# Optimization experiments

Measured on AMD Instinct MI355X. Metric: run time of the kernel, lower is better.

Reference implementation:

```python
import jax, jax.numpy as jnp
import numpy as np


def setup_inputs() -> dict:
    key = jax.random.key(0)
    k1, k2, k3 = jax.random.split(key, 3)
    batch, h, num_logical, n_pairs = 2048, 128, 64, 512
    # P: (batch, h, h) soft assignment (approximately doubly stochastic via row softmax)
    P = jax.nn.softmax(jax.random.uniform(k1, (batch, h, h), dtype=jnp.float32) * 4.0, axis=-1)
    # d_error: (h, h) precomputed nonnegative error-distance matrix, symmetric w/ zero diag
    d = jax.random.uniform(k2, (h, h), dtype=jnp.float32)
    d_error = (d + d.T) * (1.0 - jnp.eye(h, dtype=jnp.float32))
    circuit_edge_pairs = jax.random.randint(k3, (n_pairs, 2), 0, num_logical, dtype=jnp.int64)
    return {"P": P, "d_error": d_error, "circuit_edge_pairs": circuit_edge_pairs, "num_logical": num_logical}


def reference(P, d_error, circuit_edge_pairs, num_logical):
    # Restrict to logical-qubit rows, then gather both endpoints of every circuit edge.
    P_logical = P[:, :num_logical, :]                      # (b, L, h)
    P_i = P_logical[:, circuit_edge_pairs[:, 0], :]        # (b, E, h)
    P_j = P_logical[:, circuit_edge_pairs[:, 1], :]        # (b, E, h)
    # cost[b,e] = sum_{p,q} P_i[b,e,p] * d_error[p,q] * P_j[b,e,q]
    cost = jnp.einsum('bep,pq,beq->be', P_i, d_error, P_j)
    # sum_e mean_b(cost) / E == mean over (b, e)
    return jnp.mean(cost)
```

## Files before the change

kernel.cpp:

```cpp
#include <hip/hip_runtime.h>
#include <hip/hip_bf16.h>

#define B_TOTAL 2048
#define H 128
#define NL 64
#define NPAIRS 512

typedef __attribute__((ext_vector_type(8))) short bf16x8;
typedef __attribute__((ext_vector_type(4))) float f32x4;

static __device__ __forceinline__ ushort f2bf(float f) {
    uint u = __float_as_uint(f);
    u += 0x7fffu + ((u >> 16) & 1u);
    return (ushort)(u >> 16);
}
static __device__ __forceinline__ uint pk2bf(float x, float y) {
    return (uint)f2bf(x) | ((uint)f2bf(y) << 16);
}

__global__ void prep_kernel(const int* __restrict__ pairs,
                            const float* __restrict__ Dsrc,
                            float* __restrict__ Sf,
                            ushort* __restrict__ Dbf) {
    const int tid = threadIdx.x;
    if (blockIdx.x == 0) {
        __shared__ int cnt[NL * NL];
        for (int k = tid; k < NL * NL; k += 256) cnt[k] = 0;
        __syncthreads();
        for (int e = tid; e < NPAIRS; e += 256) {
            int i = pairs[2 * e] & (NL - 1);
            int j = pairs[2 * e + 1] & (NL - 1);
            atomicAdd(&cnt[i * NL + j], 1);
        }
        __syncthreads();
        for (int k = tid; k < NL * NL; k += 256) Sf[k] = (float)cnt[k];
    } else {
        int k = (blockIdx.x - 1) * 256 + tid;
        Dbf[k] = f2bf(Dsrc[k]);
    }
}

__global__ __launch_bounds__(256, 3)
void edge_loss_v4(const float* __restrict__ P,
                  const float* __restrict__ Sf,
                  const ushort* __restrict__ Dbf,
                  float* __restrict__ partials) {
    __shared__ __align__(16) ushort Ab[NL * H];
    __shared__ __align__(16) ushort Ub[NL * H];
    __shared__ float wsum[4];

    const int tid  = threadIdx.x;
    const int lane = tid & 63;
    const int w    = tid >> 6;
    const int l15  = lane & 15;
    const int lg   = lane >> 4;
    const uint rmask = (uint)l15 << 4;
    const int b    = blockIdx.x;

    float4 pf[8];
    {
        const float4* src = reinterpret_cast<const float4*>(P + (size_t)b * H * H);
#pragma unroll
        for (int k = 0; k < 8; ++k) pf[k] = src[tid + k * 256];
    }

    bf16x8 dreg[2][4];
#pragma unroll
    for (int c2 = 0; c2 < 2; ++c2) {
        const int drow = (2 * w + c2) * 16 + l15;
#pragma unroll
        for (int ks = 0; ks < 4; ++ks)
            dreg[c2][ks] = *reinterpret_cast<const bf16x8*>(Dbf + drow * H + ks * 32 + lg * 8);
    }

    float sreg[4][4];
#pragma unroll
    for (int nt = 0; nt < 4; ++nt)
#pragma unroll
        for (int r = 0; r < 4; ++r)
            sreg[nt][r] = Sf[(16 * w + 4 * lg + r) * NL + nt * 16 + l15];

#pragma unroll
    for (int k = 0; k < 8; ++k) {
        const int f4 = tid + k * 256;
        const int i  = f4 >> 5;
        const uint cb = (uint)(f4 & 31) * 8;
        uint2 d2;
        d2.x = pk2bf(pf[k].x, pf[k].y);
        d2.y = pk2bf(pf[k].z, pf[k].w);
        *reinterpret_cast<uint2*>((char*)Ab + i * 256 + (cb ^ ((uint)(i & 15) << 4))) = d2;
    }
    __syncthreads();

    f32x4 u[4][2];
#pragma unroll
    for (int it = 0; it < 4; ++it) { u[it][0] = (f32x4)0.0f; u[it][1] = (f32x4)0.0f; }
#pragma unroll
    for (int ks = 0; ks < 4; ++ks) {
        const uint koff = (uint)(ks * 64 + lg * 16);
#pragma unroll
        for (int it = 0; it < 4; ++it) {
            bf16x8 a = *reinterpret_cast<const bf16x8*>((const char*)Ab + (it * 16 + l15) * 256 + (koff ^ rmask));
            u[it][0] = __builtin_amdgcn_mfma_f32_16x16x32_bf16(a, dreg[0][ks], u[it][0], 0, 0, 0);
            u[it][1] = __builtin_amdgcn_mfma_f32_16x16x32_bf16(a, dreg[1][ks], u[it][1], 0, 0, 0);
        }
    }
#pragma unroll
    for (int it = 0; it < 4; ++it)
#pragma unroll
        for (int c2 = 0; c2 < 2; ++c2)
#pragma unroll
            for (int r = 0; r < 4; ++r) {
                const int row = it * 16 + 4 * lg + r;
                const uint cb = (uint)((2 * w + c2) * 16 + l15) * 2;
                *reinterpret_cast<ushort*>((char*)Ub + row * 256 + (cb ^ ((uint)(row & 15) << 4))) = f2bf(u[it][c2][r]);
            }
    __syncthreads();

    f32x4 m[4];
#pragma unroll
    for (int nt = 0; nt < 4; ++nt) m[nt] = (f32x4)0.0f;
#pragma unroll
    for (int ks = 0; ks < 4; ++ks) {
        const uint koff = (uint)(ks * 64 + lg * 16);
        bf16x8 a2 = *reinterpret_cast<const bf16x8*>((const char*)Ub + (16 * w + l15) * 256 + (koff ^ rmask));
#pragma unroll
        for (int nt = 0; nt < 4; ++nt) {
            bf16x8 bfr = *reinterpret_cast<const bf16x8*>((const char*)Ab + (nt * 16 + l15) * 256 + (koff ^ rmask));
            m[nt] = __builtin_amdgcn_mfma_f32_16x16x32_bf16(a2, bfr, m[nt], 0, 0, 0);
        }
    }

    float s = 0.0f;
#pragma unroll
    for (int nt = 0; nt < 4; ++nt)
#pragma unroll
        for (int r = 0; r < 4; ++r) s = fmaf(m[nt][r], sreg[nt][r], s);
#pragma unroll
    for (int off = 32; off > 0; off >>= 1) s += __shfl_down(s, off, 64);

    if (lane == 0) wsum[w] = s;
    __syncthreads();
    if (tid == 0) partials[b] = wsum[0] + wsum[1] + wsum[2] + wsum[3];
}

__global__ void finish_kernel(const float* __restrict__ partials,
                              float* __restrict__ out) {
    __shared__ float wsum[4];
    const int tid = threadIdx.x, lane = tid & 63, w = tid >> 6;
    const float4* p4 = reinterpret_cast<const float4*>(partials);
    float s = 0.0f;
#pragma unroll
    for (int k = 0; k < 2; ++k) {
        float4 v = p4[tid + k * 256];
        s += v.x + v.y + v.z + v.w;
    }
#pragma unroll
    for (int off = 32; off > 0; off >>= 1) s += __shfl_down(s, off, 64);
    if (lane == 0) wsum[w] = s;
    __syncthreads();
    if (tid == 0)
        out[0] = (wsum[0] + wsum[1] + wsum[2] + wsum[3]) *
                 (1.0f / ((float)B_TOTAL * (float)NPAIRS));
}

extern "C" void kernel_launch(void* const* d_in, const int* in_sizes, int n_in,
                              void* d_out, int out_size, void* d_ws, size_t ws_size,
                              hipStream_t stream) {
    const float* P     = (const float*)d_in[0];
    const float* Dsrc  = (const float*)d_in[1];
    const int*   pairs = (const int*)d_in[2];
    float* out = (float*)d_out;

    float*  Sf       = (float*)d_ws;
    ushort* Dbf      = (ushort*)((char*)d_ws + NL * NL * 4);
    float*  partials = (float*)((char*)d_ws + NL * NL * 4 + H * H * 2);

    prep_kernel<<<65, 256, 0, stream>>>(pairs, Dsrc, Sf, Dbf);
    edge_loss_v4<<<B_TOTAL, 256, 0, stream>>>(P, Sf, Dbf, partials);
    finish_kernel<<<1, 256, 0, stream>>>(partials, out);
}
```

Measured before the change: 184.5 us.

## Fuse prep into main kernel and process four batches per block with double-buffered loads

Removes the separate prep kernel: each block now converts d_error to bf16 and builds the pair-count matrix in LDS itself. Each block handles four batch elements, prefetching the next P slice into registers while computing the current one and storing it to a second LDS buffer, so the global load overlaps MFMA work. This amortizes D/S setup across batches and saves one launch. In exchange each block redoes the histogram and D conversion, LDS per block grows, and fewer blocks (512) give less parallelism with lower occupancy bounds.

After: 185.5 us, median of 2. Within noise of the previous version (+0.5%).

```diff
diff --git a/kernel.cpp b/kernel.cpp
--- a/kernel.cpp
+++ b/kernel.cpp
@@ -5,6 +5,8 @@
 #define H 128
 #define NL 64
 #define NPAIRS 512
+#define BPB 4
+#define NBLOCKS (B_TOTAL / BPB)
 
 typedef __attribute__((ext_vector_type(8))) short bf16x8;
 typedef __attribute__((ext_vector_type(4))) float f32x4;
@@ -18,35 +20,16 @@
     return (uint)f2bf(x) | ((uint)f2bf(y) << 16);
 }
 
-__global__ void prep_kernel(const int* __restrict__ pairs,
-                            const float* __restrict__ Dsrc,
-                            float* __restrict__ Sf,
-                            ushort* __restrict__ Dbf) {
-    const int tid = threadIdx.x;
-    if (blockIdx.x == 0) {
-        __shared__ int cnt[NL * NL];
-        for (int k = tid; k < NL * NL; k += 256) cnt[k] = 0;
-        __syncthreads();
-        for (int e = tid; e < NPAIRS; e += 256) {
-            int i = pairs[2 * e] & (NL - 1);
-            int j = pairs[2 * e + 1] & (NL - 1);
-            atomicAdd(&cnt[i * NL + j], 1);
-        }
-        __syncthreads();
-        for (int k = tid; k < NL * NL; k += 256) Sf[k] = (float)cnt[k];
-    } else {
-        int k = (blockIdx.x - 1) * 256 + tid;
-        Dbf[k] = f2bf(Dsrc[k]);
-    }
-}
-
-__global__ __launch_bounds__(256, 3)
-void edge_loss_v4(const float* __restrict__ P,
-                  const float* __restrict__ Sf,
-                  const ushort* __restrict__ Dbf,
+__global__ __launch_bounds__(256, 2)
+void edge_loss_v5(const float* __restrict__ P,
+                  const float* __restrict__ Dsrc,
+                  const int* __restrict__ pairs,
                   float* __restrict__ partials) {
-    __shared__ __align__(16) ushort Ab[NL * H];
-    __shared__ __align__(16) ushort Ub[NL * H];
+    __shared__ __align__(16) char lds_raw[49152];
+    ushort* Ab0  = (ushort*)lds_raw;
+    ushort* Ab1  = (ushort*)(lds_raw + 16384);
+    ushort* Ub   = (ushort*)(lds_raw + 32768);
+    int*    Sint = (int*)(lds_raw + 32768);
     __shared__ float wsum[4];
 
     const int tid  = threadIdx.x;
@@ -55,80 +38,112 @@
     const int l15  = lane & 15;
     const int lg   = lane >> 4;
     const uint rmask = (uint)l15 << 4;
-    const int b    = blockIdx.x;
+    const int b0   = blockIdx.x * BPB;
 
     float4 pf[8];
-    {
-        const float4* src = reinterpret_cast<const float4*>(P + (size_t)b * H * H);
+    auto loadA = [&](int b) {
+        const float4* s = reinterpret_cast<const float4*>(P + (size_t)b * H * H);
 #pragma unroll
-        for (int k = 0; k < 8; ++k) pf[k] = src[tid + k * 256];
-    }
+        for (int k = 0; k < 8; ++k) pf[k] = s[tid + k * 256];
+    };
+    auto cvtStore = [&](ushort* dst) {
+#pragma unroll
+        for (int k = 0; k < 8; ++k) {
+            const int  f4 = tid + k * 256;
+            const int  i  = f4 >> 5;
+            const uint cb = (uint)(f4 & 31) * 8;
+            uint2 d2;
+            d2.x = pk2bf(pf[k].x, pf[k].y);
+            d2.y = pk2bf(pf[k].z, pf[k].w);
+            *reinterpret_cast<uint2*>((char*)dst + i * 256 + (cb ^ ((uint)(i & 15) << 4))) = d2;
+        }
+    };
+
+    loadA(b0);
 
     bf16x8 dreg[2][4];
 #pragma unroll
     for (int c2 = 0; c2 < 2; ++c2) {
         const int drow = (2 * w + c2) * 16 + l15;
 #pragma unroll
-        for (int ks = 0; ks < 4; ++ks)
-            dreg[c2][ks] = *reinterpret_cast<const bf16x8*>(Dbf + drow * H + ks * 32 + lg * 8);
+        for (int ks = 0; ks < 4; ++ks) {
+            const float* dp = Dsrc + (size_t)drow * H + ks * 32 + lg * 8;
+            float4 x = *reinterpret_cast<const float4*>(dp);
+            float4 y = *reinterpret_cast<const float4*>(dp + 4);
+            uint4 u4;
+            u4.x = pk2bf(x.x, x.y); u4.y = pk2bf(x.z, x.w);
+            u4.z = pk2bf(y.x, y.y); u4.w = pk2bf(y.z, y.w);
+            dreg[c2][ks] = __builtin_bit_cast(bf16x8, u4);
+        }
     }
 
+#pragma unroll
+    for (int k = 0; k < 16; ++k) Sint[tid + k * 256] = 0;
+    __syncthreads();
+    {
+        int4 pr = reinterpret_cast<const int4*>(pairs)[tid];
+        atomicAdd(&Sint[(pr.x & (NL - 1)) * NL + (pr.y & (NL - 1))], 1);
+        atomicAdd(&Sint[(pr.z & (NL - 1)) * NL + (pr.w & (NL - 1))], 1);
+    }
+    __syncthreads();
     float sreg[4][4];
 #pragma unroll
     for (int nt = 0; nt < 4; ++nt)
 #pragma unroll
         for (int r = 0; r < 4; ++r)
-            sreg[nt][r] = Sf[(16 * w + 4 * lg + r) * NL + nt * 16 + l15];
-
-#pragma unroll
-    for (int k = 0; k < 8; ++k) {
-        const int f4 = tid + k * 256;
-        const int i  = f4 >> 5;
-        const uint cb = (uint)(f4 & 31) * 8;
-        uint2 d2;
-        d2.x = pk2bf(pf[k].x, pf[k].y);
-        d2.y = pk2bf(pf[k].z, pf[k].w);
-        *reinterpret_cast<uint2*>((char*)Ab + i * 256 + (cb ^ ((uint)(i & 15) << 4))) = d2;
-    }
+            sreg[nt][r] = (float)Sint[(16 * w + 4 * lg + r) * NL + nt * 16 + l15];
     __syncthreads();
 
-    f32x4 u[4][2];
-#pragma unroll
-    for (int it = 0; it < 4; ++it) { u[it][0] = (f32x4)0.0f; u[it][1] = (f32x4)0.0f; }
-#pragma unroll
-    for (int ks = 0; ks < 4; ++ks) {
-        const uint koff = (uint)(ks * 64 + lg * 16);
-#pragma unroll
-        for (int it = 0; it < 4; ++it) {
-            bf16x8 a = *reinterpret_cast<const bf16x8*>((const char*)Ab + (it * 16 + l15) * 256 + (koff ^ rmask));
-            u[it][0] = __builtin_amdgcn_mfma_f32_16x16x32_bf16(a, dreg[0][ks], u[it][0], 0, 0, 0);
-            u[it][1] = __builtin_amdgcn_mfma_f32_16x16x32_bf16(a, dreg[1][ks], u[it][1], 0, 0, 0);
-        }
-    }
-#pragma unroll
-    for (int it = 0; it < 4; ++it)
-#pragma unroll
-        for (int c2 = 0; c2 < 2; ++c2)
-#pragma unroll
-            for (int r = 0; r < 4; ++r) {
-                const int row = it * 16 + 4 * lg + r;
-                const uint cb = (uint)((2 * w + c2) * 16 + l15) * 2;
-                *reinterpret_cast<ushort*>((char*)Ub + row * 256 + (cb ^ ((uint)(row & 15) << 4))) = f2bf(u[it][c2][r]);
-            }
+    cvtStore(Ab0);
     __syncthreads();
 
     f32x4 m[4];
 #pragma unroll
     for (int nt = 0; nt < 4; ++nt) m[nt] = (f32x4)0.0f;
+
 #pragma unroll
-    for (int ks = 0; ks < 4; ++ks) {
-        const uint koff = (uint)(ks * 64 + lg * 16);
-        bf16x8 a2 = *reinterpret_cast<const bf16x8*>((const char*)Ub + (16 * w + l15) * 256 + (koff ^ rmask));
+    for (int bb = 0; bb < BPB; ++bb) {
+        ushort* Acur = (bb & 1) ? Ab1 : Ab0;
+        ushort* Anxt = (bb & 1) ? Ab0 : Ab1;
+        if (bb + 1 < BPB) loadA(b0 + bb + 1);
+
+        f32x4 u[4][2];
 #pragma unroll
-        for (int nt = 0; nt < 4; ++nt) {
-            bf16x8 bfr = *reinterpret_cast<const bf16x8*>((const char*)Ab + (nt * 16 + l15) * 256 + (koff ^ rmask));
-            m[nt] = __builtin_amdgcn_mfma_f32_16x16x32_bf16(a2, bfr, m[nt], 0, 0, 0);
+        for (int it = 0; it < 4; ++it) { u[it][0] = (f32x4)0.0f; u[it][1] = (f32x4)0.0f; }
+#pragma unroll
+        for (int ks = 0; ks < 4; ++ks) {
+            const uint koff = (uint)(ks * 64 + lg * 16);
+#pragma unroll
+            for (int it = 0; it < 4; ++it) {
+                bf16x8 a = *reinterpret_cast<const bf16x8*>((const char*)Acur + (it * 16 + l15) * 256 + (koff ^ rmask));
+                u[it][0] = __builtin_amdgcn_mfma_f32_16x16x32_bf16(a, dreg[0][ks], u[it][0], 0, 0, 0);
+                u[it][1] = __builtin_amdgcn_mfma_f32_16x16x32_bf16(a, dreg[1][ks], u[it][1], 0, 0, 0);
+            }
         }
+#pragma unroll
+        for (int it = 0; it < 4; ++it)
+#pragma unroll
+            for (int c2 = 0; c2 < 2; ++c2)
+#pragma unroll
+                for (int r = 0; r < 4; ++r) {
+                    const int  row = it * 16 + 4 * lg + r;
+                    const uint cb  = (uint)((2 * w + c2) * 16 + l15) * 2;
+                    *reinterpret_cast<ushort*>((char*)Ub + row * 256 + (cb ^ ((uint)(row & 15) << 4))) = f2bf(u[it][c2][r]);
+                }
+        __syncthreads();
+
+#pragma unroll
+        for (int ks = 0; ks < 4; ++ks) {
+            const uint koff = (uint)(ks * 64 + lg * 16);
+            bf16x8 a2 = *reinterpret_cast<const bf16x8*>((const char*)Ub + (16 * w + l15) * 256 + (koff ^ rmask));
+#pragma unroll
+            for (int nt = 0; nt < 4; ++nt) {
+                bf16x8 bfr = *reinterpret_cast<const bf16x8*>((const char*)Acur + (nt * 16 + l15) * 256 + (koff ^ rmask));
+                m[nt] = __builtin_amdgcn_mfma_f32_16x16x32_bf16(a2, bfr, m[nt], 0, 0, 0);
+            }
+        }
+        if (bb + 1 < BPB) cvtStore(Anxt);
+        __syncthreads();
     }
 
     float s = 0.0f;
@@ -141,20 +156,15 @@
 
     if (lane == 0) wsum[w] = s;
     __syncthreads();
-    if (tid == 0) partials[b] = wsum[0] + wsum[1] + wsum[2] + wsum[3];
+    if (tid == 0) partials[blockIdx.x] = wsum[0] + wsum[1] + wsum[2] + wsum[3];
 }
 
 __global__ void finish_kernel(const float* __restrict__ partials,
                               float* __restrict__ out) {
     __shared__ float wsum[4];
     const int tid = threadIdx.x, lane = tid & 63, w = tid >> 6;
-    const float4* p4 = reinterpret_cast<const float4*>(partials);
-    float s = 0.0f;
-#pragma unroll
-    for (int k = 0; k < 2; ++k) {
-        float4 v = p4[tid + k * 256];
-        s += v.x + v.y + v.z + v.w;
-    }
+    float2 v = reinterpret_cast<const float2*>(partials)[tid];
+    float s = v.x + v.y;
 #pragma unroll
     for (int off = 32; off > 0; off >>= 1) s += __shfl_down(s, off, 64);
     if (lane == 0) wsum[w] = s;
@@ -172,11 +182,8 @@
     const int*   pairs = (const int*)d_in[2];
     float* out = (float*)d_out;
 
-    float*  Sf       = (float*)d_ws;
-    ushort* Dbf      = (ushort*)((char*)d_ws + NL * NL * 4);
-    float*  partials = (float*)((char*)d_ws + NL * NL * 4 + H * H * 2);
+    float* partials = (float*)d_ws;
 
-    prep_kernel<<<65, 256, 0, stream>>>(pairs, Dsrc, Sf, Dbf);
-    edge_loss_v4<<<B_TOTAL, 256, 0, stream>>>(P, Sf, Dbf, partials);
+    edge_loss_v5<<<NBLOCKS, 256, 0, stream>>>(P, Dsrc, pairs, partials);
     finish_kernel<<<1, 256, 0, stream>>>(partials, out);
 }
```
